# Performance work log

Measured on AMD Instinct MI355X. Metric: run time of the kernel, lower is better.

Reference implementation:

```python
import jax, jax.numpy as jnp
import numpy as np

# tiny-cuda-nn canonical 2D image hash-grid config
L = 16            # n_levels
F = 2             # n_features_per_level
T = 1 << 19       # hashmap size per level
BASE = 16         # base_resolution
SCALE = 1.5       # per_level_scale
HIDDEN = 64
ENC_DIM = L * F   # 32
OUT = 3           # rgb
S = 1024          # img_res / output_size
PRIME_Y = np.uint32(2654435761)


def setup_inputs() -> dict:
    key = jax.random.key(0)
    k1, k2, k3, k4 = jax.random.split(key, 4)
    # pixel-center grid exactly as in the torch module
    half = 0.5 / S
    xs = jnp.linspace(half, 1.0 - half, S, dtype=jnp.float32)
    xv, yv = jnp.meshgrid(xs, xs, indexing='ij')
    xy = jnp.stack([yv.flatten(), xv.flatten()], axis=1)  # [S*S, 2]
    # tcnn initializes hash tables ~ U(-1e-4, 1e-4)
    hash_tables = jax.random.uniform(k1, (L, T, F), jnp.float32, -1e-4, 1e-4)
    W0 = jax.random.normal(k2, (ENC_DIM, HIDDEN), jnp.float32) * np.sqrt(2.0 / ENC_DIM)
    W1 = jax.random.normal(k3, (HIDDEN, HIDDEN), jnp.float32) * np.sqrt(2.0 / HIDDEN)
    W2 = jax.random.normal(k4, (HIDDEN, OUT), jnp.float32) * np.sqrt(2.0 / HIDDEN)
    return {"xy": xy, "hash_tables": hash_tables, "W0": W0, "W1": W1, "W2": W2}


def _encode(xy, hash_tables):
    # multiresolution hash-grid encoding with bilinear interpolation
    resolutions = jnp.floor(BASE * SCALE ** jnp.arange(L)).astype(jnp.int32)  # [L]
    offs = jnp.array([[0, 0], [0, 1], [1, 0], [1, 1]], jnp.int32)            # [4,2]

    def level(table, res):
        pos = xy * res.astype(xy.dtype)            # [N,2]
        p0 = jnp.floor(pos).astype(jnp.int32)
        w = pos - p0                                # frac weights [N,2]
        corners = p0[:, None, :] + offs[None]       # [N,4,2]
        # hashed index (tcnn spatial hash): x*1 ^ y*PRIME, mod T
        cu = corners.astype(jnp.uint32)
        hidx = ((cu[..., 0] ^ (cu[..., 1] * PRIME_Y)) % np.uint32(T)).astype(jnp.int32)
        # dense index when the grid fits in the table
        didx = corners[..., 0] + corners[..., 1] * (res + 1)
        idx = jnp.where((res + 1) * (res + 1) <= T, didx, hidx)  # [N,4]
        f = table[idx]                               # [N,4,F] gather
        wx, wy = w[:, 0:1], w[:, 1:2]
        wts = jnp.stack([(1 - wx) * (1 - wy), (1 - wx) * wy,
                         wx * (1 - wy), wx * wy], axis=1)  # [N,4,1]
        return jnp.sum(f * wts, axis=1)              # [N,F]

    feats = jax.vmap(level, in_axes=(0, 0), out_axes=1)(hash_tables, resolutions)  # [N,L,F]
    return feats.reshape(feats.shape[0], ENC_DIM)


def reference(xy, hash_tables, W0, W1, W2):
    enc = _encode(xy, hash_tables)                  # [N,32]
    h = jax.nn.relu(enc @ W0)                       # tiny MLP, no bias (FullyFusedMLP)
    h = jax.nn.relu(h @ W1)
    out = h @ W2                                    # [N,3], linear output
    return out.reshape(S, S, OUT).transpose(2, 0, 1)  # [3,S,S]
```

## Files before the change

kernel.cpp:

```cpp
#include <hip/hip_runtime.h>
#include <cstdint>
#include <cstddef>

#define S_DIM 1024
#define NPTS (S_DIM * S_DIM)
#define NLEV 16
#define TBL (1u << 19)
#define TMASK (TBL - 1u)
#define PRIME_Y 2654435761u

typedef float v4f __attribute__((ext_vector_type(4)));
typedef short v8s __attribute__((ext_vector_type(8)));

__device__ __forceinline__ void split2(float a, float b, uint32_t& hi, uint32_t& lo) {
    uint32_t ua = __float_as_uint(a), ub = __float_as_uint(b);
    uint32_t ha = ua & 0xFFFF0000u, hb = ub & 0xFFFF0000u;
    float la = a - __uint_as_float(ha);
    float lb = b - __uint_as_float(hb);
    hi = (ha >> 16) | hb;
    lo = (__float_as_uint(la) >> 16) | (__float_as_uint(lb) & 0xFFFF0000u);
}

__global__ __launch_bounds__(256) void prep_weights(const float* __restrict__ W0,
                                                    const float* __restrict__ W1,
                                                    uint4* __restrict__ ws) {
    const int tid = threadIdx.x;
    const int lane = tid & 63;
    const int m = lane & 15, q = lane >> 4;

    {
        const int tile = tid >> 6;
        const int n = tile * 16 + m;
        uint32_t hi[4], lo[4];
        #pragma unroll
        for (int d = 0; d < 4; ++d) {
            const int k0 = q * 8 + 2 * d;
            split2(W0[k0 * 64 + n], W0[(k0 + 1) * 64 + n], hi[d], lo[d]);
        }
        ws[tid]       = make_uint4(hi[0], hi[1], hi[2], hi[3]);
        ws[256 + tid] = make_uint4(lo[0], lo[1], lo[2], lo[3]);
    }

    #pragma unroll
    for (int rep = 0; rep < 2; ++rep) {
        const int unit = tid + rep * 256;
        const int l2 = unit & 63, frag = unit >> 6;
        const int nt = frag >> 1, ks = frag & 1;
        const int mm = l2 & 15, qq = l2 >> 4;
        const int n = nt * 16 + mm;
        uint32_t hi[4], lo[4];
        #pragma unroll
        for (int d = 0; d < 4; ++d) {
            const int k0 = ks * 32 + qq * 8 + 2 * d;
            split2(W1[k0 * 64 + n], W1[(k0 + 1) * 64 + n], hi[d], lo[d]);
        }
        ws[512 + unit]  = make_uint4(hi[0], hi[1], hi[2], hi[3]);
        ws[1024 + unit] = make_uint4(lo[0], lo[1], lo[2], lo[3]);
    }
}

static __device__ __forceinline__ float2 level_feat(float x, float y, int res,
                                                    const float* __restrict__ tb) {
    const float fr = (float)res;
    const float px = x * fr, py = y * fr;
    const float fx = floorf(px), fy = floorf(py);
    const float wx = px - fx, wy = py - fy;
    const int x0 = (int)fx, y0 = (int)fy;

    int i00, i01, i10, i11;
    const bool dense = ((long long)(res + 1) * (long long)(res + 1) <= (long long)TBL);
    if (dense) {
        const int st = res + 1;
        i00 = x0 + y0 * st;
        i01 = i00 + st;
        i10 = i00 + 1;
        i11 = i01 + 1;
    } else {
        const unsigned a = (unsigned)x0, b = (unsigned)y0;
        const unsigned hb0 = b * PRIME_Y;
        const unsigned hb1 = (b + 1u) * PRIME_Y;
        i00 = (int)((a ^ hb0) & TMASK);
        i01 = (int)((a ^ hb1) & TMASK);
        i10 = (int)(((a + 1u) ^ hb0) & TMASK);
        i11 = (int)(((a + 1u) ^ hb1) & TMASK);
    }

    const float2 f00 = *(const float2*)(tb + 2 * (size_t)i00);
    const float2 f01 = *(const float2*)(tb + 2 * (size_t)i01);
    const float2 f10 = *(const float2*)(tb + 2 * (size_t)i10);
    const float2 f11 = *(const float2*)(tb + 2 * (size_t)i11);

    const float omx = 1.f - wx, omy = 1.f - wy;
    const float w00 = omx * omy, w01 = omx * wy, w10 = wx * omy, w11 = wx * wy;

    float2 e;
    e.x = f00.x * w00 + f01.x * w01 + f10.x * w10 + f11.x * w11;
    e.y = f00.y * w00 + f01.y * w01 + f10.y * w10 + f11.y * w11;
    return e;
}

__global__ __launch_bounds__(256, 2) void ngp_mfma(
    const float* __restrict__ xy,
    const float* __restrict__ tables,
    const float* __restrict__ W2,
    const uint4* __restrict__ ws,
    float* __restrict__ out)
{
    __shared__ alignas(16) uint32_t encLDS[256 * 36];
    __shared__ alignas(16) uint32_t h0LDS[4 * 16 * 68];
    __shared__ alignas(16) float w2t[3 * 64];

    const int tid = threadIdx.x;
    const int lane = tid & 63;
    const int wave = tid >> 6;
    const int m = lane & 15, q = lane >> 4;
    const int blockBase = blockIdx.x * 256;

    if (tid < 192) w2t[(tid % 3) * 64 + (tid / 3)] = W2[tid];

    {
        const int pid = blockBase + tid;
        const float2 p = ((const float2*)xy)[pid];
        constexpr int RES[NLEV] = {16, 24, 36, 54, 81, 121, 182, 273,
                                   410, 615, 922, 1383, 2075, 3113, 4670, 7006};
        float enc[32];
        #pragma unroll
        for (int l = 0; l < NLEV; ++l) {
            const float* tb = tables + (size_t)l * (size_t)(TBL * 2u);
            const float2 e = level_feat(p.x, p.y, RES[l], tb);
            enc[2 * l] = e.x;
            enc[2 * l + 1] = e.y;
        }
        uint32_t hi[16], lo[16];
        #pragma unroll
        for (int d = 0; d < 16; ++d) split2(enc[2 * d], enc[2 * d + 1], hi[d], lo[d]);
        uint32_t* row = encLDS + tid * 36;
        #pragma unroll
        for (int i = 0; i < 4; ++i) {
            *((uint4*)(row + 4 * i))      = make_uint4(hi[4*i], hi[4*i+1], hi[4*i+2], hi[4*i+3]);
            *((uint4*)(row + 16 + 4 * i)) = make_uint4(lo[4*i], lo[4*i+1], lo[4*i+2], lo[4*i+3]);
        }
    }

    __syncthreads();

    v8s w0h[4], w0l[4], w1h[8], w1l[8];
    #pragma unroll
    for (int t = 0; t < 4; ++t) {
        w0h[t] = __builtin_bit_cast(v8s, ws[t * 64 + lane]);
        w0l[t] = __builtin_bit_cast(v8s, ws[256 + t * 64 + lane]);
    }
    #pragma unroll
    for (int f = 0; f < 8; ++f) {
        w1h[f] = __builtin_bit_cast(v8s, ws[512 + f * 64 + lane]);
        w1l[f] = __builtin_bit_cast(v8s, ws[1024 + f * 64 + lane]);
    }

    #pragma unroll 1
    for (int t = 0; t < 4; ++t) {
        const uint32_t* erow = encLDS + (wave * 64 + t * 16 + m) * 36;
        const v8s eH = __builtin_bit_cast(v8s, *((const uint4*)(erow + q * 4)));
        const v8s eL = __builtin_bit_cast(v8s, *((const uint4*)(erow + 16 + q * 4)));

        v4f acc0[4];
        #pragma unroll
        for (int nt = 0; nt < 4; ++nt) {
            v4f c = {0.f, 0.f, 0.f, 0.f};
            c = __builtin_amdgcn_mfma_f32_16x16x32_bf16(w0l[nt], eH, c, 0, 0, 0);
            c = __builtin_amdgcn_mfma_f32_16x16x32_bf16(w0h[nt], eL, c, 0, 0, 0);
            c = __builtin_amdgcn_mfma_f32_16x16x32_bf16(w0h[nt], eH, c, 0, 0, 0);
            acc0[nt] = c;
        }

        uint32_t* hrow = h0LDS + (wave * 16 + m) * 68;
        #pragma unroll
        for (int nt = 0; nt < 4; ++nt) {
            const float r0 = fmaxf(acc0[nt][0], 0.f), r1 = fmaxf(acc0[nt][1], 0.f);
            const float r2 = fmaxf(acc0[nt][2], 0.f), r3 = fmaxf(acc0[nt][3], 0.f);
            uint32_t h0w, l0w, h1w, l1w;
            split2(r0, r1, h0w, l0w);
            split2(r2, r3, h1w, l1w);
            *((uint2*)(hrow + nt * 8 + q * 2))      = make_uint2(h0w, h1w);
            *((uint2*)(hrow + 32 + nt * 8 + q * 2)) = make_uint2(l0w, l1w);
        }

        const v8s b0H = __builtin_bit_cast(v8s, *((const uint4*)(hrow + q * 4)));
        const v8s b0L = __builtin_bit_cast(v8s, *((const uint4*)(hrow + 32 + q * 4)));
        const v8s b1H = __builtin_bit_cast(v8s, *((const uint4*)(hrow + 16 + q * 4)));
        const v8s b1L = __builtin_bit_cast(v8s, *((const uint4*)(hrow + 48 + q * 4)));

        v4f acc1[4];
        #pragma unroll
        for (int nt = 0; nt < 4; ++nt) {
            v4f c = {0.f, 0.f, 0.f, 0.f};
            c = __builtin_amdgcn_mfma_f32_16x16x32_bf16(w1l[nt*2+0], b0H, c, 0, 0, 0);
            c = __builtin_amdgcn_mfma_f32_16x16x32_bf16(w1h[nt*2+0], b0L, c, 0, 0, 0);
            c = __builtin_amdgcn_mfma_f32_16x16x32_bf16(w1h[nt*2+0], b0H, c, 0, 0, 0);
            c = __builtin_amdgcn_mfma_f32_16x16x32_bf16(w1l[nt*2+1], b1H, c, 0, 0, 0);
            c = __builtin_amdgcn_mfma_f32_16x16x32_bf16(w1h[nt*2+1], b1L, c, 0, 0, 0);
            c = __builtin_amdgcn_mfma_f32_16x16x32_bf16(w1h[nt*2+1], b1H, c, 0, 0, 0);
            acc1[nt] = c;
        }

        float o0 = 0.f, o1 = 0.f, o2 = 0.f;
        #pragma unroll
        for (int nt = 0; nt < 4; ++nt) {
            const int n = nt * 16 + q * 4;
            const float4 wa = *((const float4*)(w2t + 0 * 64 + n));
            const float4 wb = *((const float4*)(w2t + 1 * 64 + n));
            const float4 wc = *((const float4*)(w2t + 2 * 64 + n));
            const float h0r = fmaxf(acc1[nt][0], 0.f), h1r = fmaxf(acc1[nt][1], 0.f);
            const float h2r = fmaxf(acc1[nt][2], 0.f), h3r = fmaxf(acc1[nt][3], 0.f);
            o0 = fmaf(h0r, wa.x, fmaf(h1r, wa.y, fmaf(h2r, wa.z, fmaf(h3r, wa.w, o0))));
            o1 = fmaf(h0r, wb.x, fmaf(h1r, wb.y, fmaf(h2r, wb.z, fmaf(h3r, wb.w, o1))));
            o2 = fmaf(h0r, wc.x, fmaf(h1r, wc.y, fmaf(h2r, wc.z, fmaf(h3r, wc.w, o2))));
        }
        o0 += __shfl_xor(o0, 16); o0 += __shfl_xor(o0, 32);
        o1 += __shfl_xor(o1, 16); o1 += __shfl_xor(o1, 32);
        o2 += __shfl_xor(o2, 16); o2 += __shfl_xor(o2, 32);

        if (lane < 16) {
            const int p = blockBase + wave * 64 + t * 16 + lane;
            out[p] = o0;
            out[NPTS + p] = o1;
            out[2 * NPTS + p] = o2;
        }
    }
}

extern "C" void kernel_launch(void* const* d_in, const int* in_sizes, int n_in,
                              void* d_out, int out_size, void* d_ws, size_t ws_size,
                              hipStream_t stream) {
    const float* xy     = (const float*)d_in[0];
    const float* tables = (const float*)d_in[1];
    const float* W0     = (const float*)d_in[2];
    const float* W1     = (const float*)d_in[3];
    const float* W2     = (const float*)d_in[4];
    float* out = (float*)d_out;
    uint4* ws  = (uint4*)d_ws;

    hipLaunchKernelGGL(prep_weights, dim3(1), dim3(256), 0, stream, W0, W1, ws);
    hipLaunchKernelGGL(ngp_mfma, dim3(NPTS / 256), dim3(256), 0, stream,
                       xy, tables, W2, ws, out);
}
```

Baseline: 177.8 us.

## Compute hash encoding directly in MFMA fragment layout and stage W1 in LDS

Removes the encoding staging buffer in LDS. Each lane now computes the four levels and points that its MFMA B-fragment slot needs, inside the tile loop, with per-lane level parameters and branch-free selection between dense and hashed indices. W1 fragments move from registers into LDS, the W1 and W2 passes are fused per n-tile, and launch bounds are raised to three blocks per CU to reduce register pressure and raise occupancy. The cost is less memory-level parallelism per iteration, since the gathers are now split across four loop trips. Each gather instruction also mixes four levels across lanes, which may hurt cache locality.

```diff
diff --git a/kernel.cpp b/kernel.cpp
--- a/kernel.cpp
+++ b/kernel.cpp
@@ -59,31 +59,28 @@
     }
 }
 
-static __device__ __forceinline__ float2 level_feat(float x, float y, int res,
-                                                    const float* __restrict__ tb) {
-    const float fr = (float)res;
+static __device__ __forceinline__ float2 level_feat_rt(float x, float y, float fr,
+                                                       int st , bool dense,
+                                                       const float* __restrict__ tb) {
     const float px = x * fr, py = y * fr;
     const float fx = floorf(px), fy = floorf(py);
     const float wx = px - fx, wy = py - fy;
     const int x0 = (int)fx, y0 = (int)fy;
 
-    int i00, i01, i10, i11;
-    const bool dense = ((long long)(res + 1) * (long long)(res + 1) <= (long long)TBL);
-    if (dense) {
-        const int st = res + 1;
-        i00 = x0 + y0 * st;
-        i01 = i00 + st;
-        i10 = i00 + 1;
-        i11 = i01 + 1;
-    } else {
-        const unsigned a = (unsigned)x0, b = (unsigned)y0;
-        const unsigned hb0 = b * PRIME_Y;
-        const unsigned hb1 = (b + 1u) * PRIME_Y;
-        i00 = (int)((a ^ hb0) & TMASK);
-        i01 = (int)((a ^ hb1) & TMASK);
-        i10 = (int)(((a + 1u) ^ hb0) & TMASK);
-        i11 = (int)(((a + 1u) ^ hb1) & TMASK);
-    }
+    const int d00 = x0 + y0 * st;
+    const int d01 = d00 + st;
+    const unsigned a = (unsigned)x0, b = (unsigned)y0;
+    const unsigned hb0 = b * PRIME_Y;
+    const unsigned hb1 = hb0 + PRIME_Y;
+    const int h00 = (int)((a ^ hb0) & TMASK);
+    const int h01 = (int)((a ^ hb1) & TMASK);
+    const int h10 = (int)(((a + 1u) ^ hb0) & TMASK);
+    const int h11 = (int)(((a + 1u) ^ hb1) & TMASK);
+
+    const int i00 = dense ? d00 : h00;
+    const int i01 = dense ? d01 : h01;
+    const int i10 = dense ? (d00 + 1) : h10;
+    const int i11 = dense ? (d01 + 1) : h11;
 
     const float2 f00 = *(const float2*)(tb + 2 * (size_t)i00);
     const float2 f01 = *(const float2*)(tb + 2 * (size_t)i01);
@@ -99,14 +96,14 @@
     return e;
 }
 
-__global__ __launch_bounds__(256, 2) void ngp_mfma(
+__global__ __launch_bounds__(256, 3) void ngp_mfma(
     const float* __restrict__ xy,
     const float* __restrict__ tables,
     const float* __restrict__ W2,
     const uint4* __restrict__ ws,
     float* __restrict__ out)
 {
-    __shared__ alignas(16) uint32_t encLDS[256 * 36];
+    __shared__ uint4 w1LDS[1024];
     __shared__ alignas(16) uint32_t h0LDS[4 * 16 * 68];
     __shared__ alignas(16) float w2t[3 * 64];
 
@@ -115,52 +112,49 @@
     const int wave = tid >> 6;
     const int m = lane & 15, q = lane >> 4;
     const int blockBase = blockIdx.x * 256;
-
+    const int pbase = blockBase + wave * 64 + m;
+
+    #pragma unroll
+    for (int r = 0; r < 4; ++r) w1LDS[r * 256 + tid] = ws[512 + r * 256 + tid];
     if (tid < 192) w2t[(tid % 3) * 64 + (tid / 3)] = W2[tid];
 
-    {
-        const int pid = blockBase + tid;
-        const float2 p = ((const float2*)xy)[pid];
-        constexpr int RES[NLEV] = {16, 24, 36, 54, 81, 121, 182, 273,
-                                   410, 615, 922, 1383, 2075, 3113, 4670, 7006};
-        float enc[32];
-        #pragma unroll
-        for (int l = 0; l < NLEV; ++l) {
-            const float* tb = tables + (size_t)l * (size_t)(TBL * 2u);
-            const float2 e = level_feat(p.x, p.y, RES[l], tb);
-            enc[2 * l] = e.x;
-            enc[2 * l + 1] = e.y;
-        }
-        uint32_t hi[16], lo[16];
-        #pragma unroll
-        for (int d = 0; d < 16; ++d) split2(enc[2 * d], enc[2 * d + 1], hi[d], lo[d]);
-        uint32_t* row = encLDS + tid * 36;
-        #pragma unroll
-        for (int i = 0; i < 4; ++i) {
-            *((uint4*)(row + 4 * i))      = make_uint4(hi[4*i], hi[4*i+1], hi[4*i+2], hi[4*i+3]);
-            *((uint4*)(row + 16 + 4 * i)) = make_uint4(lo[4*i], lo[4*i+1], lo[4*i+2], lo[4*i+3]);
-        }
+    float2 pc[4];
+    #pragma unroll
+    for (int t = 0; t < 4; ++t) pc[t] = ((const float2*)xy)[pbase + t * 16];
+
+    v8s w0h[4], w0l[4];
+    #pragma unroll
+    for (int t4 = 0; t4 < 4; ++t4) {
+        w0h[t4] = __builtin_bit_cast(v8s, ws[t4 * 64 + lane]);
+        w0l[t4] = __builtin_bit_cast(v8s, ws[256 + t4 * 64 + lane]);
+    }
+
+    constexpr float RESF[NLEV] = {16.f, 24.f, 36.f, 54.f, 81.f, 121.f, 182.f, 273.f,
+                                  410.f, 615.f, 922.f, 1383.f, 2075.f, 3113.f, 4670.f, 7006.f};
+    float frs[4]; int sts[4]; bool dns[4]; const float* tbs[4];
+    #pragma unroll
+    for (int i = 0; i < 4; ++i) {
+        const float fAB = (q & 1) ? RESF[4 + i] : RESF[i];
+        const float fCD = (q & 1) ? RESF[12 + i] : RESF[8 + i];
+        const float f = (q & 2) ? fCD : fAB;
+        frs[i] = f;
+        sts[i] = (int)f + 1;
+        dns[i] = (i < 2) ? (q <= 2) : (q <= 1);
+        tbs[i] = tables + ((size_t)(unsigned)(q * 4 + i) << 20);
     }
 
     __syncthreads();
-
-    v8s w0h[4], w0l[4], w1h[8], w1l[8];
-    #pragma unroll
-    for (int t = 0; t < 4; ++t) {
-        w0h[t] = __builtin_bit_cast(v8s, ws[t * 64 + lane]);
-        w0l[t] = __builtin_bit_cast(v8s, ws[256 + t * 64 + lane]);
-    }
-    #pragma unroll
-    for (int f = 0; f < 8; ++f) {
-        w1h[f] = __builtin_bit_cast(v8s, ws[512 + f * 64 + lane]);
-        w1l[f] = __builtin_bit_cast(v8s, ws[1024 + f * 64 + lane]);
-    }
 
     #pragma unroll 1
     for (int t = 0; t < 4; ++t) {
-        const uint32_t* erow = encLDS + (wave * 64 + t * 16 + m) * 36;
-        const v8s eH = __builtin_bit_cast(v8s, *((const uint4*)(erow + q * 4)));
-        const v8s eL = __builtin_bit_cast(v8s, *((const uint4*)(erow + 16 + q * 4)));
+        uint32_t ehd[4], eld[4];
+        #pragma unroll
+        for (int i = 0; i < 4; ++i) {
+            const float2 e = level_feat_rt(pc[t].x, pc[t].y, frs[i], sts[i], dns[i], tbs[i]);
+            split2(e.x, e.y, ehd[i], eld[i]);
+        }
+        const v8s eH = __builtin_bit_cast(v8s, make_uint4(ehd[0], ehd[1], ehd[2], ehd[3]));
+        const v8s eL = __builtin_bit_cast(v8s, make_uint4(eld[0], eld[1], eld[2], eld[3]));
 
         v4f acc0[4];
         #pragma unroll
@@ -189,32 +183,32 @@
         const v8s b1H = __builtin_bit_cast(v8s, *((const uint4*)(hrow + 16 + q * 4)));
         const v8s b1L = __builtin_bit_cast(v8s, *((const uint4*)(hrow + 48 + q * 4)));
 
-        v4f acc1[4];
+        float o0 = 0.f, o1 = 0.f, o2 = 0.f;
         #pragma unroll
         for (int nt = 0; nt < 4; ++nt) {
+            const v8s a0h = __builtin_bit_cast(v8s, w1LDS[(nt * 2 + 0) * 64 + lane]);
+            const v8s a0l = __builtin_bit_cast(v8s, w1LDS[512 + (nt * 2 + 0) * 64 + lane]);
+            const v8s a1h = __builtin_bit_cast(v8s, w1LDS[(nt * 2 + 1) * 64 + lane]);
+            const v8s a1l = __builtin_bit_cast(v8s, w1LDS[512 + (nt * 2 + 1) * 64 + lane]);
             v4f c = {0.f, 0.f, 0.f, 0.f};
-            c = __builtin_amdgcn_mfma_f32_16x16x32_bf16(w1l[nt*2+0], b0H, c, 0, 0, 0);
-            c = __builtin_amdgcn_mfma_f32_16x16x32_bf16(w1h[nt*2+0], b0L, c, 0, 0, 0);
-            c = __builtin_amdgcn_mfma_f32_16x16x32_bf16(w1h[nt*2+0], b0H, c, 0, 0, 0);
-            c = __builtin_amdgcn_mfma_f32_16x16x32_bf16(w1l[nt*2+1], b1H, c, 0, 0, 0);
-            c = __builtin_amdgcn_mfma_f32_16x16x32_bf16(w1h[nt*2+1], b1L, c, 0, 0, 0);
-            c = __builtin_amdgcn_mfma_f32_16x16x32_bf16(w1h[nt*2+1], b1H, c, 0, 0, 0);
-            acc1[nt] = c;
-        }
-
-        float o0 = 0.f, o1 = 0.f, o2 = 0.f;
-        #pragma unroll
-        for (int nt = 0; nt < 4; ++nt) {
+            c = __builtin_amdgcn_mfma_f32_16x16x32_bf16(a0l, b0H, c, 0, 0, 0);
+            c = __builtin_amdgcn_mfma_f32_16x16x32_bf16(a0h, b0L, c, 0, 0, 0);
+            c = __builtin_amdgcn_mfma_f32_16x16x32_bf16(a0h, b0H, c, 0, 0, 0);
+            c = __builtin_amdgcn_mfma_f32_16x16x32_bf16(a1l, b1H, c, 0, 0, 0);
+            c = __builtin_amdgcn_mfma_f32_16x16x32_bf16(a1h, b1L, c, 0, 0, 0);
+            c = __builtin_amdgcn_mfma_f32_16x16x32_bf16(a1h, b1H, c, 0, 0, 0);
+
             const int n = nt * 16 + q * 4;
             const float4 wa = *((const float4*)(w2t + 0 * 64 + n));
             const float4 wb = *((const float4*)(w2t + 1 * 64 + n));
             const float4 wc = *((const float4*)(w2t + 2 * 64 + n));
-            const float h0r = fmaxf(acc1[nt][0], 0.f), h1r = fmaxf(acc1[nt][1], 0.f);
-            const float h2r = fmaxf(acc1[nt][2], 0.f), h3r = fmaxf(acc1[nt][3], 0.f);
+            const float h0r = fmaxf(c[0], 0.f), h1r = fmaxf(c[1], 0.f);
+            const float h2r = fmaxf(c[2], 0.f), h3r = fmaxf(c[3], 0.f);
             o0 = fmaf(h0r, wa.x, fmaf(h1r, wa.y, fmaf(h2r, wa.z, fmaf(h3r, wa.w, o0))));
             o1 = fmaf(h0r, wb.x, fmaf(h1r, wb.y, fmaf(h2r, wb.z, fmaf(h3r, wb.w, o1))));
             o2 = fmaf(h0r, wc.x, fmaf(h1r, wc.y, fmaf(h2r, wc.z, fmaf(h3r, wc.w, o2))));
         }
+
         o0 += __shfl_xor(o0, 16); o0 += __shfl_xor(o0, 32);
         o1 += __shfl_xor(o1, 16); o1 += __shfl_xor(o1, 32);
         o2 += __shfl_xor(o2, 16); o2 += __shfl_xor(o2, 32);
```

Result: slower. 280.9 us (+58.0%).
